# Optimization experiments

Measured on AMD Instinct MI355X. Metric: run time of the kernel, lower is better.

Reference implementation:

```python
import jax, jax.numpy as jnp
import numpy as np

B, C, H, W = 32, 128, 56, 56
CMAX, OUT, KS, K = 128, 256, 3, 4
HID = 64  # attn_fc hidden width


def setup_inputs() -> dict:
    key = jax.random.key(0)
    ks = jax.random.split(key, 6)
    x = jax.random.normal(ks[0], (B, C, H, W), dtype=jnp.float32)
    weight_bank = jax.random.normal(ks[1], (K, OUT, CMAX, KS, KS), dtype=jnp.float32)
    fc1_w = jax.random.normal(ks[2], (HID, CMAX), dtype=jnp.float32) * (1.0 / np.sqrt(CMAX))
    fc1_b = jnp.zeros((HID,), dtype=jnp.float32)
    fc2_w = jax.random.normal(ks[3], (K, HID), dtype=jnp.float32) * (1.0 / np.sqrt(HID))
    fc2_b = jnp.zeros((K,), dtype=jnp.float32)
    return {"x": x, "weight_bank": weight_bank, "fc1_w": fc1_w, "fc1_b": fc1_b,
            "fc2_w": fc2_w, "fc2_b": fc2_b}


def reference(x, weight_bank, fc1_w, fc1_b, fc2_w, fc2_b):
    b, c, h, w = x.shape
    # AdaptiveAvgPool2d(1) on zero-channel-padded input -> mean over HW, pad channel dim
    pooled = jnp.mean(x, axis=(2, 3))                       # [B, C]
    pooled = jnp.pad(pooled, ((0, 0), (0, CMAX - c)))       # [B, CMAX]
    hdn = jax.nn.relu(pooled @ fc1_w.T + fc1_b)             # [B, 64]
    attn = jax.nn.softmax(hdn @ fc2_w.T + fc2_b, axis=-1)   # [B, K]
    # per-sample kernel synthesis
    weight = jnp.einsum('bk,kocij->bocij', attn, weight_bank[:, :, :c])  # [B,O,C,k,k]
    # single grouped conv instead of B separate conv launches
    lhs = x.reshape(1, b * c, h, w)
    rhs = weight.reshape(b * OUT, c, KS, KS)
    p = KS // 2
    out = jax.lax.conv_general_dilated(
        lhs, rhs, window_strides=(1, 1), padding=[(p, p), (p, p)],
        feature_group_count=b,
        dimension_numbers=('NCHW', 'OIHW', 'NCHW'))
    return out.reshape(b, OUT, h, w)
```

## Files before the change

kernel.cpp:

```cpp
#include <hip/hip_runtime.h>
#include <hip/hip_bf16.h>

#define B_    32
#define C_    128
#define H_    56
#define W_    56
#define OUT_  256
#define K_    4
#define HID_  64
#define HW_   (H_*W_)
#define KV_   (C_*9)
#define PH_   58
#define PW_   58
#define PP_   (PH_*PW_)

typedef __attribute__((ext_vector_type(8))) short short8_t;
typedef __attribute__((ext_vector_type(4))) float float4_t;

typedef __hip_bfloat16 bf16;

__device__ __forceinline__ short f2bf(float v) {
    union { bf16 h; short s; } u; u.h = __float2bfloat16(v); return u.s;
}

typedef __attribute__((address_space(1))) const unsigned int* gas_t;
typedef __attribute__((address_space(3))) unsigned int* las_t;

__device__ __forceinline__ void gl_lds16(const short* g, short* l) {
    __builtin_amdgcn_global_load_lds((gas_t)(const void*)g, (las_t)(void*)l, 16, 0, 0);
}

__global__ __launch_bounds__(256) void dc_pool(const float* __restrict__ x,
                                               float* __restrict__ pooled) {
    int bc = blockIdx.x;
    const float4_t* xp = (const float4_t*)(x + (size_t)bc * HW_);
    float s = 0.f;
    for (int j = threadIdx.x; j < HW_/4; j += 256) {
        float4_t v = xp[j];
        s += v[0] + v[1] + v[2] + v[3];
    }
    #pragma unroll
    for (int off = 32; off; off >>= 1) s += __shfl_down(s, off, 64);
    __shared__ float ps[4];
    if ((threadIdx.x & 63) == 0) ps[threadIdx.x >> 6] = s;
    __syncthreads();
    if (threadIdx.x == 0) pooled[bc] = ps[0] + ps[1] + ps[2] + ps[3];
}

__global__ __launch_bounds__(256) void dc_xt(const float* __restrict__ x,
                                             short* __restrict__ xTp) {
    int b = blockIdx.y, n0 = blockIdx.x * 128;
    __shared__ short t[C_][130];
    for (int i = threadIdx.x; i < C_*128; i += 256) {
        int c = i >> 7, nn = i & 127;
        int pp = n0 + nn;
        int py = pp / PW_, px = pp - py*PW_;
        bool valid = (pp < PP_) & (py >= 1) & (py <= H_) & (px >= 1) & (px <= W_);
        float v = valid ? x[((size_t)b*C_ + c)*HW_ + (py-1)*W_ + (px-1)] : 0.f;
        t[c][nn] = f2bf(v);
    }
    __syncthreads();
    typedef __attribute__((ext_vector_type(2))) unsigned int uint2_t;
    for (int i = threadIdx.x; i < 32*128; i += 256) {
        int nn = i >> 5, c4 = (i & 31) * 4;
        int pp = n0 + nn;
        if (pp < PP_) {
            union { unsigned short u[4]; uint2_t v; } pk;
            pk.u[0] = (unsigned short)t[c4  ][nn];
            pk.u[1] = (unsigned short)t[c4+1][nn];
            pk.u[2] = (unsigned short)t[c4+2][nn];
            pk.u[3] = (unsigned short)t[c4+3][nn];
            *(uint2_t*)&xTp[((size_t)b*PP_ + pp)*C_ + c4] = pk.v;
        }
    }
}

__global__ __launch_bounds__(64) void dc_attn(const float* __restrict__ pooled,
                                              const float* __restrict__ fc1w,
                                              const float* __restrict__ fc1b,
                                              const float* __restrict__ fc2w,
                                              const float* __restrict__ fc2b,
                                              float* __restrict__ attn) {
    int b = blockIdx.x, h = threadIdx.x;
    __shared__ float pl[C_];
    __shared__ float hdn[HID_];
    __shared__ float logit[K_];
    pl[h]      = pooled[b*C_ + h]      * (1.0f / HW_);
    pl[h + 64] = pooled[b*C_ + 64 + h] * (1.0f / HW_);
    __syncthreads();
    float s = fc1b[h];
    #pragma unroll 8
    for (int c = 0; c < C_; ++c) s += pl[c] * fc1w[h*C_ + c];
    hdn[h] = fmaxf(s, 0.f);
    __syncthreads();
    if (h < K_) {
        float t = fc2b[h];
        #pragma unroll 8
        for (int j = 0; j < HID_; ++j) t += hdn[j] * fc2w[h*HID_ + j];
        logit[h] = t;
    }
    __syncthreads();
    if (h == 0) {
        float m = fmaxf(fmaxf(logit[0], logit[1]), fmaxf(logit[2], logit[3]));
        float e0 = __expf(logit[0]-m), e1 = __expf(logit[1]-m);
        float e2 = __expf(logit[2]-m), e3 = __expf(logit[3]-m);
        float inv = 1.0f / (e0+e1+e2+e3);
        attn[b*K_+0]=e0*inv; attn[b*K_+1]=e1*inv;
        attn[b*K_+2]=e2*inv; attn[b*K_+3]=e3*inv;
    }
}

__global__ __launch_bounds__(256) void dc_wsynth(const float* __restrict__ bank,
                                                 const float* __restrict__ attn,
                                                 bf16* __restrict__ Ws) {
    int o = blockIdx.x;
    int b0 = blockIdx.y * 8;
    __shared__ float wb[4*KV_];
    for (int i = threadIdx.x; i < 4*KV_; i += 256) {
        int kk = i / KV_, r = i - kk*KV_;
        wb[i] = bank[((size_t)kk*OUT_ + o)*KV_ + r];
    }
    __syncthreads();
    for (int bi = 0; bi < 8; ++bi) {
        int b = b0 + bi;
        float a0 = attn[b*K_+0], a1 = attn[b*K_+1];
        float a2 = attn[b*K_+2], a3 = attn[b*K_+3];
        unsigned* dst = (unsigned*)&Ws[((size_t)b*OUT_ + o)*KV_];
        for (int ii = threadIdx.x; ii < KV_/2; ii += 256) {
            int i0 = 2*ii;
            int tap0 = i0 >> 7, c0 = i0 & 127;
            int i1 = i0 + 1;
            int tap1 = i1 >> 7, c1 = i1 & 127;
            float v0 = a0*wb[c0*9+tap0] + a1*wb[KV_+c0*9+tap0]
                     + a2*wb[2*KV_+c0*9+tap0] + a3*wb[3*KV_+c0*9+tap0];
            float v1 = a0*wb[c1*9+tap1] + a1*wb[KV_+c1*9+tap1]
                     + a2*wb[2*KV_+c1*9+tap1] + a3*wb[3*KV_+c1*9+tap1];
            union { unsigned short u[2]; unsigned v; } pk;
            pk.u[0] = (unsigned short)f2bf(v0);
            pk.u[1] = (unsigned short)f2bf(v1);
            dst[ii] = pk.v;
        }
    }
}

__global__ __launch_bounds__(256) void dc_gemm(const short* __restrict__ Ws,
                                               const short* __restrict__ xTp,
                                               float* __restrict__ out) {
    const int b  = blockIdx.z;
    const int m0 = blockIdx.y * 128;
    const int n0 = blockIdx.x * 128;
    const int tid  = threadIdx.x;
    const int lane = tid & 63;
    const int wv   = tid >> 6;
    const int wm   = wv & 1, wn = wv >> 1;
    const int l16  = lane & 15, quad = lane >> 4;

    __shared__ short lA[128*64];
    __shared__ short lB[128*64];

    const short* aG[4];
    const short* bG[4];
    short* aL[4];
    short* bL[4];
    #pragma unroll
    for (int j = 0; j < 4; ++j) {
        int t = 4*wv + j;
        int row = (t >> 1) * 16 + l16;
        int kq  = t & 1;
        aG[j] = Ws + ((size_t)b*OUT_ + m0 + row)*KV_ + kq*32 + quad*8;
        int n = n0 + row;
        int idc = min(n, HW_ - 1);
        int y = idc / W_, xx2 = idc - y * W_;
        int pbc = (y + 1) * PW_ + (xx2 + 1);
        bG[j] = xTp + ((size_t)b*PP_ + pbc)*C_ + kq*32 + quad*8;
        aL[j] = lA + t*512;
        bL[j] = lB + t*512;
    }

    int nidx[4];
    #pragma unroll
    for (int ni = 0; ni < 4; ++ni)
        nidx[ni] = n0 + wn*64 + ni*16 + l16;

    float4_t acc[4][4];
    #pragma unroll
    for (int mi = 0; mi < 4; ++mi)
        #pragma unroll
        for (int ni = 0; ni < 4; ++ni)
            acc[mi][ni] = (float4_t){0.f, 0.f, 0.f, 0.f};

    for (int tap = 0; tap < 9; ++tap) {
        int ty = tap / 3, tx = tap - 3*ty;
        int doff = (ty - 1) * PW_ + (tx - 1);
        #pragma unroll
        for (int half = 0; half < 2; ++half) {
            const int kk = tap*128 + half*64;
            const int cc = half*64;
            #pragma unroll
            for (int j = 0; j < 4; ++j) {
                gl_lds16(aG[j] + kk, aL[j]);
                gl_lds16(bG[j] + doff*C_ + cc, bL[j]);
            }
            __syncthreads();
            #pragma unroll
            for (int kq = 0; kq < 2; ++kq) {
                short8_t af[4], bf[4];
                #pragma unroll
                for (int mi = 0; mi < 4; ++mi)
                    af[mi] = *(const short8_t*)(lA + ((wm*4+mi)*2 + kq)*512 + lane*8);
                #pragma unroll
                for (int ni = 0; ni < 4; ++ni)
                    bf[ni] = *(const short8_t*)(lB + ((wn*4+ni)*2 + kq)*512 + lane*8);
                #pragma unroll
                for (int mi = 0; mi < 4; ++mi)
                    #pragma unroll
                    for (int ni = 0; ni < 4; ++ni)
                        acc[mi][ni] = __builtin_amdgcn_mfma_f32_16x16x32_bf16(
                            af[mi], bf[ni], acc[mi][ni], 0, 0, 0);
            }
            __syncthreads();
        }
    }

    const size_t obase = (size_t)b * OUT_ * HW_;
    #pragma unroll
    for (int mi = 0; mi < 4; ++mi) {
        int m = m0 + wm*64 + mi*16 + quad*4;
        #pragma unroll
        for (int ni = 0; ni < 4; ++ni) {
            int n = nidx[ni];
            if (n < HW_) {
                float* op = out + obase + (size_t)m * HW_ + n;
                #pragma unroll
                for (int r = 0; r < 4; ++r)
                    op[(size_t)r * HW_] = acc[mi][ni][r];
            }
        }
    }
}

extern "C" void kernel_launch(void* const* d_in, const int* in_sizes, int n_in,
                              void* d_out, int out_size, void* d_ws, size_t ws_size,
                              hipStream_t stream) {
    const float* x    = (const float*)d_in[0];
    const float* bank = (const float*)d_in[1];
    const float* fc1w = (const float*)d_in[2];
    const float* fc1b = (const float*)d_in[3];
    const float* fc2w = (const float*)d_in[4];
    const float* fc2b = (const float*)d_in[5];
    float* out = (float*)d_out;

    char* ws = (char*)d_ws;
    float* pooled = (float*)ws;
    float* attn   = (float*)(ws + 16*1024);
    bf16*  Ws     = (bf16*) (ws + 32*1024);
    short* xTp    = (short*)(ws + 32*1024 + 18874368);

    dc_pool  <<<B_*C_, 256, 0, stream>>>(x, pooled);
    dc_xt    <<<dim3(27, B_), 256, 0, stream>>>(x, xTp);
    dc_attn  <<<B_,     64, 0, stream>>>(pooled, fc1w, fc1b, fc2w, fc2b, attn);
    dc_wsynth<<<dim3(OUT_, 4), 256, 0, stream>>>(bank, attn, Ws);
    dc_gemm  <<<dim3(25, 2, B_), 256, 0, stream>>>((const short*)Ws, xTp, out);
}
```

Baseline: 322.9 us.

## Double-buffer LDS stages in dc_gemm and swizzle block order across XCDs

```diff
diff --git a/kernel.cpp b/kernel.cpp
--- a/kernel.cpp
+++ b/kernel.cpp
@@ -146,35 +146,38 @@
 __global__ __launch_bounds__(256) void dc_gemm(const short* __restrict__ Ws,
                                                const short* __restrict__ xTp,
                                                float* __restrict__ out) {
-    const int b  = blockIdx.z;
-    const int m0 = blockIdx.y * 128;
-    const int n0 = blockIdx.x * 128;
+    int orig = blockIdx.x;
+    int swz  = (orig & 7) * 200 + (orig >> 3);
+    const int bx  = swz % 25;
+    const int byz = swz / 25;
+    const int by  = byz & 1;
+    const int b   = byz >> 1;
+
+    const int m0 = by * 128;
+    const int n0 = bx * 128;
     const int tid  = threadIdx.x;
     const int lane = tid & 63;
     const int wv   = tid >> 6;
     const int wm   = wv & 1, wn = wv >> 1;
     const int l16  = lane & 15, quad = lane >> 4;
 
-    __shared__ short lA[128*64];
-    __shared__ short lB[128*64];
-
-    const short* aG[4];
-    const short* bG[4];
-    short* aL[4];
-    short* bL[4];
-    #pragma unroll
-    for (int j = 0; j < 4; ++j) {
-        int t = 4*wv + j;
-        int row = (t >> 1) * 16 + l16;
-        int kq  = t & 1;
-        aG[j] = Ws + ((size_t)b*OUT_ + m0 + row)*KV_ + kq*32 + quad*8;
+    __shared__ short lA[2][4096];
+    __shared__ short lB[2][4096];
+
+    const short* aG[2];
+    const short* bG[2];
+    int tOff[2];
+    #pragma unroll
+    for (int j = 0; j < 2; ++j) {
+        int t = 2*wv + j;
+        int row = t*16 + l16;
+        aG[j] = Ws + ((size_t)b*OUT_ + m0 + row)*KV_ + quad*8;
         int n = n0 + row;
         int idc = min(n, HW_ - 1);
         int y = idc / W_, xx2 = idc - y * W_;
         int pbc = (y + 1) * PW_ + (xx2 + 1);
-        bG[j] = xTp + ((size_t)b*PP_ + pbc)*C_ + kq*32 + quad*8;
-        aL[j] = lA + t*512;
-        bL[j] = lB + t*512;
+        bG[j] = xTp + ((size_t)b*PP_ + pbc)*C_ + quad*8;
+        tOff[j] = t * 512;
     }
 
     int nidx[4];
@@ -189,37 +192,42 @@
         for (int ni = 0; ni < 4; ++ni)
             acc[mi][ni] = (float4_t){0.f, 0.f, 0.f, 0.f};
 
-    for (int tap = 0; tap < 9; ++tap) {
+    auto stage = [&](int ss, int buf) {
+        int tap = ss >> 2, kq2 = ss & 3;
         int ty = tap / 3, tx = tap - 3*ty;
-        int doff = (ty - 1) * PW_ + (tx - 1);
-        #pragma unroll
-        for (int half = 0; half < 2; ++half) {
-            const int kk = tap*128 + half*64;
-            const int cc = half*64;
+        int doff = ((ty - 1) * PW_ + (tx - 1)) * C_;
+        int ka = tap*128 + kq2*32;
+        int cb = kq2*32;
+        #pragma unroll
+        for (int j = 0; j < 2; ++j) {
+            gl_lds16(aG[j] + ka,        &lA[buf][tOff[j]]);
+            gl_lds16(bG[j] + doff + cb, &lB[buf][tOff[j]]);
+        }
+    };
+
+    auto compute = [&](int buf) {
+        short8_t af[4], bfr[4];
+        #pragma unroll
+        for (int mi = 0; mi < 4; ++mi)
+            af[mi] = *(const short8_t*)(&lA[buf][(wm*4+mi)*512 + lane*8]);
+        #pragma unroll
+        for (int ni = 0; ni < 4; ++ni)
+            bfr[ni] = *(const short8_t*)(&lB[buf][(wn*4+ni)*512 + lane*8]);
+        #pragma unroll
+        for (int mi = 0; mi < 4; ++mi)
             #pragma unroll
-            for (int j = 0; j < 4; ++j) {
-                gl_lds16(aG[j] + kk, aL[j]);
-                gl_lds16(bG[j] + doff*C_ + cc, bL[j]);
-            }
-            __syncthreads();
-            #pragma unroll
-            for (int kq = 0; kq < 2; ++kq) {
-                short8_t af[4], bf[4];
-                #pragma unroll
-                for (int mi = 0; mi < 4; ++mi)
-                    af[mi] = *(const short8_t*)(lA + ((wm*4+mi)*2 + kq)*512 + lane*8);
-                #pragma unroll
-                for (int ni = 0; ni < 4; ++ni)
-                    bf[ni] = *(const short8_t*)(lB + ((wn*4+ni)*2 + kq)*512 + lane*8);
-                #pragma unroll
-                for (int mi = 0; mi < 4; ++mi)
-                    #pragma unroll
-                    for (int ni = 0; ni < 4; ++ni)
-                        acc[mi][ni] = __builtin_amdgcn_mfma_f32_16x16x32_bf16(
-                            af[mi], bf[ni], acc[mi][ni], 0, 0, 0);
-            }
-            __syncthreads();
-        }
+            for (int ni = 0; ni < 4; ++ni)
+                acc[mi][ni] = __builtin_amdgcn_mfma_f32_16x16x32_bf16(
+                    af[mi], bfr[ni], acc[mi][ni], 0, 0, 0);
+    };
+
+    stage(0, 0);
+    __syncthreads();
+    for (int ss = 0; ss < 36; ++ss) {
+        int buf = ss & 1;
+        if (ss < 35) stage(ss + 1, buf ^ 1);
+        compute(buf);
+        __syncthreads();
     }
 
     const size_t obase = (size_t)b * OUT_ * HW_;
@@ -260,5 +268,5 @@
     dc_xt    <<<dim3(27, B_), 256, 0, stream>>>(x, xTp);
     dc_attn  <<<B_,     64, 0, stream>>>(pooled, fc1w, fc1b, fc2w, fc2b, attn);
     dc_wsynth<<<dim3(OUT_, 4), 256, 0, stream>>>(bank, attn, Ws);
-    dc_gemm  <<<dim3(25, 2, B_), 256, 0, stream>>>((const short*)Ws, xTp, out);
-}
+    dc_gemm  <<<dim3(1600), 256, 0, stream>>>((const short*)Ws, xTp, out);
+}
```

After: 321.3 us. No clear change (-0.5%).

## Fuse pooling with transpose and attention MLP into weight synthesis

Applied to the files above, without the earlier changes.

```diff
diff --git a/kernel.cpp b/kernel.cpp
--- a/kernel.cpp
+++ b/kernel.cpp
@@ -30,27 +30,31 @@
     __builtin_amdgcn_global_load_lds((gas_t)(const void*)g, (las_t)(void*)l, 16, 0, 0);
 }
 
-__global__ __launch_bounds__(256) void dc_pool(const float* __restrict__ x,
-                                               float* __restrict__ pooled) {
-    int bc = blockIdx.x;
-    const float4_t* xp = (const float4_t*)(x + (size_t)bc * HW_);
-    float s = 0.f;
-    for (int j = threadIdx.x; j < HW_/4; j += 256) {
-        float4_t v = xp[j];
-        s += v[0] + v[1] + v[2] + v[3];
-    }
-    #pragma unroll
-    for (int off = 32; off; off >>= 1) s += __shfl_down(s, off, 64);
+__global__ __launch_bounds__(256) void dc_px(const float* __restrict__ x,
+                                             short* __restrict__ xTp,
+                                             float* __restrict__ pooled) {
+    __shared__ short t[C_][130];
     __shared__ float ps[4];
-    if ((threadIdx.x & 63) == 0) ps[threadIdx.x >> 6] = s;
-    __syncthreads();
-    if (threadIdx.x == 0) pooled[bc] = ps[0] + ps[1] + ps[2] + ps[3];
-}
-
-__global__ __launch_bounds__(256) void dc_xt(const float* __restrict__ x,
-                                             short* __restrict__ xTp) {
-    int b = blockIdx.y, n0 = blockIdx.x * 128;
-    __shared__ short t[C_][130];
+    int idx = blockIdx.x;
+
+    if (idx < B_*C_) {
+        const float4_t* xp = (const float4_t*)(x + (size_t)idx * HW_);
+        float s = 0.f;
+        for (int j = threadIdx.x; j < HW_/4; j += 256) {
+            float4_t v = xp[j];
+            s += v[0] + v[1] + v[2] + v[3];
+        }
+        #pragma unroll
+        for (int off = 32; off; off >>= 1) s += __shfl_down(s, off, 64);
+        if ((threadIdx.x & 63) == 0) ps[threadIdx.x >> 6] = s;
+        __syncthreads();
+        if (threadIdx.x == 0) pooled[idx] = ps[0] + ps[1] + ps[2] + ps[3];
+        return;
+    }
+
+    int xb = idx - B_*C_;
+    int b = xb / 27, nchunk = xb - b*27;
+    int n0 = nchunk * 128;
     for (int i = threadIdx.x; i < C_*128; i += 256) {
         int c = i >> 7, nn = i & 127;
         int pp = n0 + nn;
@@ -75,58 +79,64 @@
     }
 }
 
-__global__ __launch_bounds__(64) void dc_attn(const float* __restrict__ pooled,
-                                              const float* __restrict__ fc1w,
-                                              const float* __restrict__ fc1b,
-                                              const float* __restrict__ fc2w,
-                                              const float* __restrict__ fc2b,
-                                              float* __restrict__ attn) {
-    int b = blockIdx.x, h = threadIdx.x;
-    __shared__ float pl[C_];
-    __shared__ float hdn[HID_];
-    __shared__ float logit[K_];
-    pl[h]      = pooled[b*C_ + h]      * (1.0f / HW_);
-    pl[h + 64] = pooled[b*C_ + 64 + h] * (1.0f / HW_);
-    __syncthreads();
-    float s = fc1b[h];
-    #pragma unroll 8
-    for (int c = 0; c < C_; ++c) s += pl[c] * fc1w[h*C_ + c];
-    hdn[h] = fmaxf(s, 0.f);
-    __syncthreads();
-    if (h < K_) {
-        float t = fc2b[h];
-        #pragma unroll 8
-        for (int j = 0; j < HID_; ++j) t += hdn[j] * fc2w[h*HID_ + j];
-        logit[h] = t;
-    }
-    __syncthreads();
-    if (h == 0) {
-        float m = fmaxf(fmaxf(logit[0], logit[1]), fmaxf(logit[2], logit[3]));
-        float e0 = __expf(logit[0]-m), e1 = __expf(logit[1]-m);
-        float e2 = __expf(logit[2]-m), e3 = __expf(logit[3]-m);
-        float inv = 1.0f / (e0+e1+e2+e3);
-        attn[b*K_+0]=e0*inv; attn[b*K_+1]=e1*inv;
-        attn[b*K_+2]=e2*inv; attn[b*K_+3]=e3*inv;
-    }
-}
-
-__global__ __launch_bounds__(256) void dc_wsynth(const float* __restrict__ bank,
-                                                 const float* __restrict__ attn,
+__global__ __launch_bounds__(256) void dc_wsattn(const float* __restrict__ bank,
+                                                 const float* __restrict__ pooled,
+                                                 const float* __restrict__ fc1w,
+                                                 const float* __restrict__ fc1b,
+                                                 const float* __restrict__ fc2w,
+                                                 const float* __restrict__ fc2b,
                                                  bf16* __restrict__ Ws) {
     int o = blockIdx.x;
     int b0 = blockIdx.y * 8;
+    int tid = threadIdx.x;
     __shared__ float wb[4*KV_];
-    for (int i = threadIdx.x; i < 4*KV_; i += 256) {
-        int kk = i / KV_, r = i - kk*KV_;
-        wb[i] = bank[((size_t)kk*OUT_ + o)*KV_ + r];
-    }
-    __syncthreads();
+    __shared__ float pl[8][C_];
+    __shared__ float hdnl[8][HID_];
+    __shared__ float attn_l[8][K_];
+
+    const float4_t* bk4 = (const float4_t*)bank;
+    float4_t* wb4 = (float4_t*)wb;
+    for (int i = tid; i < KV_; i += 256) {
+        int kk = i / 288, r = i - kk*288;
+        wb4[i] = bk4[((size_t)kk*OUT_ + o)*288 + r];
+    }
+    for (int i = tid; i < 8*C_; i += 256)
+        pl[i >> 7][i & 127] = pooled[(size_t)(b0 + (i >> 7))*C_ + (i & 127)] * (1.0f/HW_);
+    __syncthreads();
+
+    #pragma unroll
+    for (int r = 0; r < 2; ++r) {
+        int p = r*256 + tid;
+        int bi = p >> 6, h = p & 63;
+        float s = fc1b[h];
+        #pragma unroll 8
+        for (int c = 0; c < C_; ++c) s += pl[bi][c] * fc1w[h*C_ + c];
+        hdnl[bi][h] = fmaxf(s, 0.f);
+    }
+    __syncthreads();
+
+    if (tid < 32) {
+        int bi = tid >> 2, k = tid & 3;
+        float t0 = fc2b[k];
+        #pragma unroll 8
+        for (int j = 0; j < HID_; ++j) t0 += hdnl[bi][j] * fc2w[k*HID_ + j];
+        float m = t0;
+        m = fmaxf(m, __shfl_xor(m, 1, 64));
+        m = fmaxf(m, __shfl_xor(m, 2, 64));
+        float e = __expf(t0 - m);
+        float se = e;
+        se += __shfl_xor(se, 1, 64);
+        se += __shfl_xor(se, 2, 64);
+        attn_l[bi][k] = e / se;
+    }
+    __syncthreads();
+
     for (int bi = 0; bi < 8; ++bi) {
         int b = b0 + bi;
-        float a0 = attn[b*K_+0], a1 = attn[b*K_+1];
-        float a2 = attn[b*K_+2], a3 = attn[b*K_+3];
+        float a0 = attn_l[bi][0], a1 = attn_l[bi][1];
+        float a2 = attn_l[bi][2], a3 = attn_l[bi][3];
         unsigned* dst = (unsigned*)&Ws[((size_t)b*OUT_ + o)*KV_];
-        for (int ii = threadIdx.x; ii < KV_/2; ii += 256) {
+        for (int ii = tid; ii < KV_/2; ii += 256) {
             int i0 = 2*ii;
             int tap0 = i0 >> 7, c0 = i0 & 127;
             int i1 = i0 + 1;
@@ -252,13 +262,11 @@
 
     char* ws = (char*)d_ws;
     float* pooled = (float*)ws;
-    float* attn   = (float*)(ws + 16*1024);
     bf16*  Ws     = (bf16*) (ws + 32*1024);
     short* xTp    = (short*)(ws + 32*1024 + 18874368);
 
-    dc_pool  <<<B_*C_, 256, 0, stream>>>(x, pooled);
-    dc_xt    <<<dim3(27, B_), 256, 0, stream>>>(x, xTp);
-    dc_attn  <<<B_,     64, 0, stream>>>(pooled, fc1w, fc1b, fc2w, fc2b, attn);
-    dc_wsynth<<<dim3(OUT_, 4), 256, 0, stream>>>(bank, attn, Ws);
+    dc_px    <<<B_*C_ + 27*B_, 256, 0, stream>>>(x, xTp, pooled);
+    dc_wsattn<<<dim3(OUT_, 4), 256, 0, stream>>>(bank, pooled, fc1w, fc1b,
+                                                 fc2w, fc2b, Ws);
     dc_gemm  <<<dim3(25, 2, B_), 256, 0, stream>>>((const short*)Ws, xTp, out);
 }
```

Measured after the change: 342.5 us. 6.1% more time.
